# Kernel optimization log

Measured on AMD Instinct MI355X. Metric: run time of the kernel, lower is better.

## Reference

```python
import jax, jax.numpy as jnp
import numpy as np

TOP_K = 32
TEMPERATURE = 1.0
PARAM_SCALE = 0.02


def setup_inputs() -> dict:
    key = jax.random.key(0)
    ks = jax.random.split(key, 7)
    B, S, D, F, P, R = 2, 1024, 1024, 4096, 256, 64
    x = jax.random.normal(ks[0], (B, S, D), dtype=jnp.float32)
    fc1_A = jax.random.normal(ks[1], (P, D, R), dtype=jnp.float32) * PARAM_SCALE
    fc1_B = jax.random.normal(ks[2], (P, R, F), dtype=jnp.float32) * PARAM_SCALE
    fc2_A = jax.random.normal(ks[3], (P, F, R), dtype=jnp.float32) * PARAM_SCALE
    fc2_B = jax.random.normal(ks[4], (P, R, D), dtype=jnp.float32) * PARAM_SCALE
    fc1_logits = jax.random.normal(ks[5], (P,), dtype=jnp.float32)
    fc2_logits = jax.random.normal(ks[6], (P,), dtype=jnp.float32)
    return {"x": x, "fc1_A": fc1_A, "fc1_B": fc1_B, "fc2_A": fc2_A,
            "fc2_B": fc2_B, "fc1_logits": fc1_logits, "fc2_logits": fc2_logits}


def _compose_weight(logits, A, B):
    """Top-k select primitives, softmax composition weights, weighted low-rank sum.

    A: (P, d_in, r), B: (P, r, d_out) -> W: (d_in, d_out)
    """
    vals, idx = jax.lax.top_k(logits, TOP_K)          # (K,), (K,)
    w = jax.nn.softmax(vals / TEMPERATURE)            # composition weights over selected
    A_sel = A[idx]                                    # (K, d_in, r) gather
    B_sel = B[idx]                                    # (K, r, d_out) gather
    return jnp.einsum('k,kir,kro->io', w, A_sel, B_sel)


def reference(x, fc1_A, fc1_B, fc2_A, fc2_B, fc1_logits, fc2_logits):
    W1 = _compose_weight(fc1_logits, fc1_A, fc1_B)    # (D, F)
    W2 = _compose_weight(fc2_logits, fc2_A, fc2_B)    # (F, D)
    h = jax.nn.gelu(jnp.einsum('bsd,df->bsf', x, W1))
    return jnp.einsum('bsf,fd->bsd', h, W2)
```

## Files before the change

### kernel.cpp

```cpp
#include <hip/hip_runtime.h>
#include <cstdint>
#include <cstddef>

typedef __attribute__((ext_vector_type(8))) short bhalf8;
typedef __attribute__((ext_vector_type(4))) float f32x4;

__device__ __forceinline__ unsigned short f2bf(float f){
    unsigned int u = __float_as_uint(f);
    u += 0x7fffu + ((u >> 16) & 1u);
    return (unsigned short)(u >> 16);
}

__device__ __forceinline__ float gelu_tanh(float x){
    const float c0 = 0.7978845608028654f;
    float x3 = x * x * x;
    float t = tanhf(c0 * (x + 0.044715f * x3));
    return 0.5f * x * (1.0f + t);
}

__global__ void topk_softmax_kernel(const float* __restrict__ lg1,
                                    const float* __restrict__ lg2,
                                    int* __restrict__ idx_out,
                                    float* __restrict__ w_out)
{
    const float* lg = (blockIdx.x == 0) ? lg1 : lg2;
    int*   idxo = idx_out + blockIdx.x * 32;
    float* wo   = w_out   + blockIdx.x * 32;
    const int lane = threadIdx.x;
    float v[4];
    #pragma unroll
    for (int j = 0; j < 4; ++j) v[j] = lg[lane * 4 + j];
    __shared__ float svals[32];
    for (int k = 0; k < 32; ++k){
        float bv = -1e30f; int bi = 0;
        #pragma unroll
        for (int j = 0; j < 4; ++j){
            if (v[j] > bv){ bv = v[j]; bi = lane * 4 + j; }
        }
        for (int off = 32; off > 0; off >>= 1){
            float ov = __shfl_down(bv, off);
            int   oi = __shfl_down(bi, off);
            if (ov > bv){ bv = ov; bi = oi; }
        }
        bv = __shfl(bv, 0);
        bi = __shfl(bi, 0);
        if (lane == 0){ svals[k] = bv; idxo[k] = bi; }
        if ((bi >> 2) == lane) v[bi & 3] = -1e30f;
    }
    if (lane == 0){
        float mx = svals[0];
        float sum = 0.f;
        for (int k = 0; k < 32; ++k){ float e = expf(svals[k] - mx); wo[k] = e; sum += e; }
        float inv = 1.f / sum;
        for (int k = 0; k < 32; ++k) wo[k] *= inv;
    }
}

__global__ void convert_bf16_kernel(const float* __restrict__ src,
                                    unsigned short* __restrict__ dst, int n4)
{
    int v = blockIdx.x * 256 + threadIdx.x;
    if (v >= n4) return;
    float4 x = ((const float4*)src)[v];
    ushort4 o; o.x = f2bf(x.x); o.y = f2bf(x.y); o.z = f2bf(x.z); o.w = f2bf(x.w);
    ((ushort4*)dst)[v] = o;
}

__global__ void gather_nat_kernel(const float* __restrict__ src,
                                  unsigned short* __restrict__ dst,
                                  const int* __restrict__ idx,
                                  const float* __restrict__ w,
                                  int Drows, int use_scale, int n4)
{
    int v = blockIdx.x * 256 + threadIdx.x;
    if (v >= n4) return;
    int c4 = v & 511;
    int d  = v >> 9;
    int k  = c4 >> 4;
    int r4 = c4 & 15;
    int p  = idx[k];
    float sc = use_scale ? w[k] : 1.0f;
    const float4* s = (const float4*)(src + ((size_t)p * Drows + d) * 64) + r4;
    float4 x = *s;
    ushort4 o;
    o.x = f2bf(sc * x.x); o.y = f2bf(sc * x.y);
    o.z = f2bf(sc * x.z); o.w = f2bf(sc * x.w);
    *(ushort4*)(dst + (size_t)d * 2048 + k * 64 + r4 * 4) = o;
}

__global__ void gather_tr_kernel(const float* __restrict__ src,
                                 unsigned short* __restrict__ dst,
                                 const int* __restrict__ idx,
                                 const float* __restrict__ w,
                                 int Fcols, int use_scale)
{
    const int k  = blockIdx.y;
    const int f0 = blockIdx.x * 64;
    const int p  = idx[k];
    const float sc = use_scale ? w[k] : 1.0f;
    __shared__ float tile[64][65];
    const int t  = threadIdx.x;
    const int cf = t & 15;
    const int r0 = t >> 4;
    #pragma unroll
    for (int pass = 0; pass < 4; ++pass){
        int r = r0 + pass * 16;
        float4 x = *((const float4*)(src + ((size_t)p * 64 + r) * Fcols + f0) + cf);
        tile[r][cf * 4 + 0] = x.x; tile[r][cf * 4 + 1] = x.y;
        tile[r][cf * 4 + 2] = x.z; tile[r][cf * 4 + 3] = x.w;
    }
    __syncthreads();
    const int r4  = t & 15;
    const int fl0 = t >> 4;
    #pragma unroll
    for (int pass = 0; pass < 4; ++pass){
        int fl = fl0 + pass * 16;
        ushort4 o;
        o.x = f2bf(sc * tile[r4 * 4 + 0][fl]);
        o.y = f2bf(sc * tile[r4 * 4 + 1][fl]);
        o.z = f2bf(sc * tile[r4 * 4 + 2][fl]);
        o.w = f2bf(sc * tile[r4 * 4 + 3][fl]);
        *(ushort4*)(dst + (size_t)(f0 + fl) * 2048 + k * 64 + r4 * 4) = o;
    }
}

template<int EPI>
__launch_bounds__(256, 2)
__global__ void gemm_nt_kernel(const unsigned short* __restrict__ A,
                               const unsigned short* __restrict__ Bt,
                               void* __restrict__ Cout,
                               int M, int N, int K)
{
    __shared__ unsigned short sA[128 * 32];
    __shared__ unsigned short sB[128 * 32];
    const int bm = blockIdx.y * 128;
    const int bn = blockIdx.x * 128;
    const int t    = threadIdx.x;
    const int wave = t >> 6;
    const int lane = t & 63;
    const int wr   = (wave >> 1) * 64;
    const int wc   = (wave & 1) * 64;
    const int m16  = lane & 15;
    const int quad = lane >> 4;
    const int srow = t >> 2;
    const int scol = t & 3;

    f32x4 acc[4][4];
    const f32x4 z = {0.f, 0.f, 0.f, 0.f};
    #pragma unroll
    for (int i = 0; i < 4; ++i)
        #pragma unroll
        for (int j = 0; j < 4; ++j) acc[i][j] = z;

    const unsigned short* Arow = A  + (size_t)(bm + srow) * K + scol * 8;
    const unsigned short* Brow = Bt + (size_t)(bn + srow) * K + scol * 8;

    for (int k0 = 0; k0 < K; k0 += 32){
        *(bhalf8*)(sA + srow * 32 + scol * 8)        = *(const bhalf8*)(Arow + k0);
        *(bhalf8*)(sA + (srow + 64) * 32 + scol * 8) = *(const bhalf8*)(Arow + (size_t)64 * K + k0);
        *(bhalf8*)(sB + srow * 32 + scol * 8)        = *(const bhalf8*)(Brow + k0);
        *(bhalf8*)(sB + (srow + 64) * 32 + scol * 8) = *(const bhalf8*)(Brow + (size_t)64 * K + k0);
        __syncthreads();

        bhalf8 af[4], bfr[4];
        #pragma unroll
        for (int i = 0; i < 4; ++i)
            af[i] = *(const bhalf8*)(sA + (wr + i * 16 + m16) * 32 + quad * 8);
        #pragma unroll
        for (int j = 0; j < 4; ++j)
            bfr[j] = *(const bhalf8*)(sB + (wc + j * 16 + m16) * 32 + quad * 8);

        #pragma unroll
        for (int i = 0; i < 4; ++i)
            #pragma unroll
            for (int j = 0; j < 4; ++j)
                acc[i][j] = __builtin_amdgcn_mfma_f32_16x16x32_bf16(af[i], bfr[j], acc[i][j], 0, 0, 0);
        __syncthreads();
    }

    #pragma unroll
    for (int i = 0; i < 4; ++i){
        #pragma unroll
        for (int j = 0; j < 4; ++j){
            #pragma unroll
            for (int r = 0; r < 4; ++r){
                int row = bm + wr + i * 16 + quad * 4 + r;
                int col = bn + wc + j * 16 + m16;
                float vv = acc[i][j][r];
                if (EPI == 1) vv = gelu_tanh(vv);
                if (EPI == 2) ((float*)Cout)[(size_t)row * N + col] = vv;
                else ((unsigned short*)Cout)[(size_t)row * N + col] = f2bf(vv);
            }
        }
    }
}

extern "C" void kernel_launch(void* const* d_in, const int* in_sizes, int n_in,
                              void* d_out, int out_size, void* d_ws, size_t ws_size,
                              hipStream_t stream)
{
    const float* x    = (const float*)d_in[0];
    const float* fc1A = (const float*)d_in[1];
    const float* fc1B = (const float*)d_in[2];
    const float* fc2A = (const float*)d_in[3];
    const float* fc2B = (const float*)d_in[4];
    const float* lg1  = (const float*)d_in[5];
    const float* lg2  = (const float*)d_in[6];
    float* out = (float*)d_out;

    char* ws = (char*)d_ws;
    int*            idxb = (int*)(ws + 0);
    float*          wb   = (float*)(ws + 256);
    unsigned short* x16  = (unsigned short*)(ws + 4096);
    unsigned short* Ag1  = (unsigned short*)(ws + 4096 + (4u << 20));
    unsigned short* Bt1  = (unsigned short*)(ws + 4096 + (8u << 20));
    unsigned short* W1t  = (unsigned short*)(ws + 4096 + (24u << 20));
    unsigned short* hbuf = (unsigned short*)(ws + 4096 + (32u << 20));
    unsigned short* Ag2  = Bt1;
    unsigned short* Bg2t = Ag1;
    unsigned short* W2t  = W1t;

    topk_softmax_kernel<<<dim3(2), dim3(64), 0, stream>>>(lg1, lg2, idxb, wb);

    convert_bf16_kernel<<<dim3(2048), dim3(256), 0, stream>>>(x, x16, 524288);

    gather_nat_kernel<<<dim3(2048), dim3(256), 0, stream>>>(fc1A, Ag1, idxb, wb, 1024, 1, 524288);
    gather_tr_kernel<<<dim3(64, 32), dim3(256), 0, stream>>>(fc1B, Bt1, idxb, wb, 4096, 0);

    gemm_nt_kernel<0><<<dim3(8, 32), dim3(256), 0, stream>>>(Bt1, Ag1, W1t, 4096, 1024, 2048);

    gemm_nt_kernel<1><<<dim3(32, 16), dim3(256), 0, stream>>>(x16, W1t, hbuf, 2048, 4096, 1024);

    gather_nat_kernel<<<dim3(8192), dim3(256), 0, stream>>>(fc2A, Ag2, idxb + 32, wb + 32, 4096, 0, 2097152);
    gather_tr_kernel<<<dim3(16, 32), dim3(256), 0, stream>>>(fc2B, Bg2t, idxb + 32, wb + 32, 1024, 1);

    gemm_nt_kernel<0><<<dim3(32, 8), dim3(256), 0, stream>>>(Bg2t, Ag2, W2t, 1024, 4096, 2048);

    gemm_nt_kernel<2><<<dim3(8, 16), dim3(256), 0, stream>>>(hbuf, W2t, out, 2048, 1024, 4096);
}
```

Baseline: 699.3 us.

## Split-K the final GEMM with atomics and use async global-to-LDS loads

The final hidden-by-W2 GEMM is split four ways along K, so 512 blocks run instead of 128 on a GPU with many CUs. Partial sums go into the output with float atomicAdd, which needs a new zero-fill kernel before everything else. All GEMM tile loads now go straight from global memory into LDS via global_load_lds, skipping the register round-trip. The cost is extra atomic traffic on the output, a nondeterministic summation order, and reliance on the compiler inserting the right waits before the barrier.

```diff
diff --git a/kernel.cpp b/kernel.cpp
--- a/kernel.cpp
+++ b/kernel.cpp
@@ -16,6 +16,12 @@
     float x3 = x * x * x;
     float t = tanhf(c0 * (x + 0.044715f * x3));
     return 0.5f * x * (1.0f + t);
+}
+
+__device__ __forceinline__ void async_lds16(const unsigned short* g, unsigned short* l){
+    __builtin_amdgcn_global_load_lds(
+        (const __attribute__((address_space(1))) void*)g,
+        (__attribute__((address_space(3))) void*)l, 16, 0, 0);
 }
 
 __global__ void topk_softmax_kernel(const float* __restrict__ lg1,
@@ -64,6 +70,12 @@
     float4 x = ((const float4*)src)[v];
     ushort4 o; o.x = f2bf(x.x); o.y = f2bf(x.y); o.z = f2bf(x.z); o.w = f2bf(x.w);
     ((ushort4*)dst)[v] = o;
+}
+
+__global__ void zero_kernel(float4* __restrict__ p, int n4)
+{
+    int v = blockIdx.x * 256 + threadIdx.x;
+    if (v < n4){ float4 z = {0.f,0.f,0.f,0.f}; p[v] = z; }
 }
 
 __global__ void gather_nat_kernel(const float* __restrict__ src,
@@ -129,7 +141,7 @@
 __global__ void gemm_nt_kernel(const unsigned short* __restrict__ A,
                                const unsigned short* __restrict__ Bt,
                                void* __restrict__ Cout,
-                               int M, int N, int K)
+                               int M, int N, int K, int Kslice)
 {
     __shared__ unsigned short sA[128 * 32];
     __shared__ unsigned short sB[128 * 32];
@@ -152,14 +164,17 @@
         #pragma unroll
         for (int j = 0; j < 4; ++j) acc[i][j] = z;
 
-    const unsigned short* Arow = A  + (size_t)(bm + srow) * K + scol * 8;
-    const unsigned short* Brow = Bt + (size_t)(bn + srow) * K + scol * 8;
-
-    for (int k0 = 0; k0 < K; k0 += 32){
-        *(bhalf8*)(sA + srow * 32 + scol * 8)        = *(const bhalf8*)(Arow + k0);
-        *(bhalf8*)(sA + (srow + 64) * 32 + scol * 8) = *(const bhalf8*)(Arow + (size_t)64 * K + k0);
-        *(bhalf8*)(sB + srow * 32 + scol * 8)        = *(const bhalf8*)(Brow + k0);
-        *(bhalf8*)(sB + (srow + 64) * 32 + scol * 8) = *(const bhalf8*)(Brow + (size_t)64 * K + k0);
+    const int kbeg = blockIdx.z * Kslice;
+    const unsigned short* Arow = A  + (size_t)(bm + srow) * K + scol * 8 + kbeg;
+    const unsigned short* Brow = Bt + (size_t)(bn + srow) * K + scol * 8 + kbeg;
+    unsigned short* lA = sA + srow * 32 + scol * 8;
+    unsigned short* lB = sB + srow * 32 + scol * 8;
+
+    for (int k0 = 0; k0 < Kslice; k0 += 32){
+        async_lds16(Arow + k0,                    lA);
+        async_lds16(Arow + (size_t)64 * K + k0,   lA + 64 * 32);
+        async_lds16(Brow + k0,                    lB);
+        async_lds16(Brow + (size_t)64 * K + k0,   lB + 64 * 32);
         __syncthreads();
 
         bhalf8 af[4], bfr[4];
@@ -188,7 +203,8 @@
                 int col = bn + wc + j * 16 + m16;
                 float vv = acc[i][j][r];
                 if (EPI == 1) vv = gelu_tanh(vv);
-                if (EPI == 2) ((float*)Cout)[(size_t)row * N + col] = vv;
+                if (EPI == 2)      ((float*)Cout)[(size_t)row * N + col] = vv;
+                else if (EPI == 3) atomicAdd(&((float*)Cout)[(size_t)row * N + col], vv);
                 else ((unsigned short*)Cout)[(size_t)row * N + col] = f2bf(vv);
             }
         }
@@ -220,6 +236,8 @@
     unsigned short* Bg2t = Ag1;
     unsigned short* W2t  = W1t;
 
+    zero_kernel<<<dim3(2048), dim3(256), 0, stream>>>((float4*)out, 524288);
+
     topk_softmax_kernel<<<dim3(2), dim3(64), 0, stream>>>(lg1, lg2, idxb, wb);
 
     convert_bf16_kernel<<<dim3(2048), dim3(256), 0, stream>>>(x, x16, 524288);
@@ -227,14 +245,14 @@
     gather_nat_kernel<<<dim3(2048), dim3(256), 0, stream>>>(fc1A, Ag1, idxb, wb, 1024, 1, 524288);
     gather_tr_kernel<<<dim3(64, 32), dim3(256), 0, stream>>>(fc1B, Bt1, idxb, wb, 4096, 0);
 
-    gemm_nt_kernel<0><<<dim3(8, 32), dim3(256), 0, stream>>>(Bt1, Ag1, W1t, 4096, 1024, 2048);
-
-    gemm_nt_kernel<1><<<dim3(32, 16), dim3(256), 0, stream>>>(x16, W1t, hbuf, 2048, 4096, 1024);
+    gemm_nt_kernel<0><<<dim3(8, 32), dim3(256), 0, stream>>>(Bt1, Ag1, W1t, 4096, 1024, 2048, 2048);
+
+    gemm_nt_kernel<1><<<dim3(32, 16), dim3(256), 0, stream>>>(x16, W1t, hbuf, 2048, 4096, 1024, 1024);
 
     gather_nat_kernel<<<dim3(8192), dim3(256), 0, stream>>>(fc2A, Ag2, idxb + 32, wb + 32, 4096, 0, 2097152);
     gather_tr_kernel<<<dim3(16, 32), dim3(256), 0, stream>>>(fc2B, Bg2t, idxb + 32, wb + 32, 1024, 1);
 
-    gemm_nt_kernel<0><<<dim3(32, 8), dim3(256), 0, stream>>>(Bg2t, Ag2, W2t, 1024, 4096, 2048);
-
-    gemm_nt_kernel<2><<<dim3(8, 16), dim3(256), 0, stream>>>(hbuf, W2t, out, 2048, 1024, 4096);
-}
+    gemm_nt_kernel<0><<<dim3(32, 8), dim3(256), 0, stream>>>(Bg2t, Ag2, W2t, 1024, 4096, 2048, 2048);
+
+    gemm_nt_kernel<3><<<dim3(8, 16, 4), dim3(256), 0, stream>>>(hbuf, W2t, out, 2048, 1024, 4096, 1024);
+}
```

Measured after the change: 664.7 us. 1.05x faster.
